# Performance work log

Measured on AMD Instinct MI355X. Metric: run time of the kernel, lower is better.

The kernel has to match this reference:

```python
import jax, jax.numpy as jnp
import numpy as np

B, S, E, H = 2, 2048, 1024, 16
D = E // H  # head_dim = 64
TRIL = D * (D + 1) // 2  # 2080


def setup_inputs() -> dict:
    key = jax.random.key(0)
    ks = jax.random.split(key, 6)
    return {
        "x": jax.random.normal(ks[0], (B, S, E), dtype=jnp.float32),
        "params": jax.random.normal(ks[1], (H, TRIL), dtype=jnp.float32),
        "Wv": jax.random.normal(ks[2], (E, E), dtype=jnp.float32) * 0.02,
        "bv": jax.random.normal(ks[3], (E,), dtype=jnp.float32) * 0.02,
        "Wo": jax.random.normal(ks[4], (E, E), dtype=jnp.float32) * 0.02,
        "bo": jax.random.normal(ks[5], (E,), dtype=jnp.float32) * 0.02,
    }


def reference(x, params, Wv, bv, Wo, bo):
    # x: [B,S,E]; 'symmetry' modification, dropout in eval mode (identity).
    bs, seq_len, emb_dim = x.shape
    d = D
    rows, cols = jnp.tril_indices(d)  # row-major, matches torch.tril_indices
    # Build per-head lower-triangular factor then symmetric PSD Wqk = L @ L^T.
    tril = jnp.zeros((H, d, d), dtype=x.dtype).at[:, rows, cols].set(params)
    Wqk = jnp.einsum('hij,hkj->hik', tril, tril)  # [H,d,d]
    xh = x.reshape(bs, seq_len, H, d)             # [B,S,H,d]
    # scores[b,h,s,t] = x_s^T Wqk_h x_t / sqrt(d)
    t = jnp.einsum('bshd,hde->bshe', xh, Wqk)
    scores = jnp.einsum('bshe,bthe->bhst', t, xh) / jnp.sqrt(jnp.asarray(d, x.dtype))
    attn = jax.nn.softmax(scores, axis=-1)        # [B,H,S,S]
    Vh = (x @ Wv.T + bv).reshape(bs, seq_len, H, d)
    out = jnp.einsum('bhst,bthd->bshd', attn, Vh).reshape(bs, seq_len, emb_dim)
    return out @ Wo.T + bo
```

## Files before the change

kernel.cpp:

```cpp
#include <hip/hip_runtime.h>
#include <math.h>

static constexpr int kB = 2;
static constexpr int kS = 2048;
static constexpr int kE = 1024;
static constexpr int kH = 16;
static constexpr int kD = 64;
static constexpr int kTRIL = 2080;

typedef __attribute__((ext_vector_type(8))) _Float16 f16x8;
typedef __attribute__((ext_vector_type(4))) _Float16 f16x4;
typedef __attribute__((ext_vector_type(2))) __fp16 fp16x2;
typedef __attribute__((ext_vector_type(4))) float f32x4;
typedef __attribute__((ext_vector_type(16))) float f32x16;
typedef __attribute__((ext_vector_type(4))) unsigned int u32x4;
typedef __attribute__((ext_vector_type(2))) unsigned int u32x2;

__device__ __forceinline__ void split_f16(float f, _Float16& hi, _Float16& lo) {
    hi = (_Float16)f;
    lo = (_Float16)(f - (float)hi);
}

__device__ __forceinline__ void gload_lds16(const void* g, void* l) {
    __builtin_amdgcn_global_load_lds(
        (const __attribute__((address_space(1))) unsigned int*)g,
        (__attribute__((address_space(3))) unsigned int*)l, 16, 0, 0);
}

__device__ __forceinline__ unsigned pack_f16(float a, float b) {
    fp16x2 p = __builtin_amdgcn_cvt_pkrtz(a, b);
    return __builtin_bit_cast(unsigned, p);
}

__device__ __forceinline__ unsigned partner32(unsigned x, int hi) {
    u32x2 r = __builtin_amdgcn_permlane32_swap(x, x, false, false);
    return hi ? r[0] : r[1];
}
__device__ __forceinline__ float partner32_f(float x, int hi) {
    return __builtin_bit_cast(float, partner32(__builtin_bit_cast(unsigned, x), hi));
}

__device__ __forceinline__ float max3f(float a, float b, float c) {
    return fmaxf(fmaxf(a, b), c);
}

__global__ __launch_bounds__(256) void setup_kernel(
    const float* __restrict__ Wv, const float* __restrict__ Wo,
    const float* __restrict__ x, const float* __restrict__ params,
    _Float16* __restrict__ wvf, _Float16* __restrict__ wof,
    _Float16* __restrict__ xf,
    _Float16* __restrict__ wqkh, _Float16* __restrict__ wqkl)
{
    const int bid = blockIdx.x;
    if (bid < 2048) {
        const int half = bid >> 10;
        const int i = (bid & 1023) * 256 + threadIdx.x;
        const float* src = half ? Wo : Wv;
        _Float16* dst = half ? wof : wvf;
        const float4 v = ((const float4*)src)[i];
        f16x4 o = {(_Float16)v.x, (_Float16)v.y, (_Float16)v.z, (_Float16)v.w};
        ((f16x4*)dst)[i] = o;
        return;
    }
    if (bid < 6144) {
        const int i = (bid - 2048) * 256 + threadIdx.x;
        const float4 v = ((const float4*)x)[i];
        f16x4 o = {(_Float16)v.x, (_Float16)v.y, (_Float16)v.z, (_Float16)v.w};
        ((f16x4*)xf)[i] = o;
        return;
    }
    __shared__ float p[kTRIL];
    const int h = bid - 6144;
    for (int i = threadIdx.x; i < kTRIL; i += 256) p[i] = params[h * kTRIL + i];
    __syncthreads();
    for (int idx = threadIdx.x; idx < kD * kD; idx += 256) {
        const int i = idx >> 6;
        const int j = idx & 63;
        const int m = i < j ? i : j;
        const float* pi = p + (i * (i + 1)) / 2;
        const float* pj = p + (j * (j + 1)) / 2;
        float s = 0.f;
        for (int k = 0; k <= m; ++k) s += pi[k] * pj[k];
        _Float16 a, b;
        split_f16(s, a, b);
        wqkh[h * kD * kD + idx] = a;
        wqkl[h * kD * kD + idx] = b;
    }
}

__global__ __launch_bounds__(256) void mid_kernel(
    const _Float16* __restrict__ xf, const _Float16* __restrict__ wvf,
    const float* __restrict__ bv, _Float16* __restrict__ VtG,
    const _Float16* __restrict__ wqkh, const _Float16* __restrict__ wqkl,
    _Float16* __restrict__ Qhf, _Float16* __restrict__ Qlf)
{
    __shared__ char arena[65536];
    const int tid = threadIdx.x;
    const int w = tid >> 6, l = tid & 63;
    const int srow = 8 * w + (l >> 3);
    const int cpos = l & 7;

    if (blockIdx.x < 256) {
        _Float16 (*Ab)[128 * 64] = (_Float16 (*)[128 * 64])arena;
        _Float16 (*Bb)[128 * 64] = (_Float16 (*)[128 * 64])(arena + 32768);
        const int K_ = kE;
        const int g = l >> 4, lm = l & 15;
        const int wm = w >> 1, wn = w & 1;
        const int bm = (blockIdx.x >> 3) * 128, bn = (blockIdx.x & 7) * 128;

        f32x4 acc[4][4];
#pragma unroll
        for (int i = 0; i < 4; ++i)
#pragma unroll
            for (int j = 0; j < 4; ++j) acc[i][j] = (f32x4){0.f, 0.f, 0.f, 0.f};

        auto stage = [&](int buf, int k0) {
#pragma unroll
            for (int j = 0; j < 4; ++j) {
                const int r = 32 * j + srow;
                const int c = cpos ^ (r & 7);
                gload_lds16(xf + (size_t)(bm + r) * K_ + k0 + c * 8, &Ab[buf][j * 2048 + w * 512]);
                gload_lds16(wvf + (size_t)(bn + r) * K_ + k0 + c * 8, &Bb[buf][j * 2048 + w * 512]);
            }
        };

        stage(0, 0);
        __syncthreads();
        int cur = 0;
        const int NT = K_ / 64;
        for (int t = 0; t < NT; ++t) {
            if (t + 1 < NT) stage(cur ^ 1, 64 * (t + 1));
            f16x8 a[4][2], bf[4][2];
#pragma unroll
            for (int i = 0; i < 4; ++i) {
                const int rA = wm * 64 + i * 16 + lm;
                const int rB = wn * 64 + i * 16 + lm;
#pragma unroll
                for (int ks = 0; ks < 2; ++ks) {
                    a[i][ks]  = *(const f16x8*)&Ab[cur][rA * 64 + (((4 * ks + g) ^ (rA & 7)) * 8)];
                    bf[i][ks] = *(const f16x8*)&Bb[cur][rB * 64 + (((4 * ks + g) ^ (rB & 7)) * 8)];
                }
            }
            __builtin_amdgcn_s_setprio(1);
#pragma unroll
            for (int ks = 0; ks < 2; ++ks)
#pragma unroll
                for (int mi = 0; mi < 4; ++mi)
#pragma unroll
                    for (int ni = 0; ni < 4; ++ni)
                        acc[mi][ni] = __builtin_amdgcn_mfma_f32_16x16x32_f16(
                            a[mi][ks], bf[ni][ks], acc[mi][ni], 0, 0, 0);
            __builtin_amdgcn_s_setprio(0);
            __syncthreads();
            cur ^= 1;
        }

#pragma unroll
        for (int ni = 0; ni < 4; ++ni) {
            const int col = bn + wn * 64 + ni * 16 + lm;
            const float bb = bv[col];
            const int hh = col >> 6, dd = col & 63;
#pragma unroll
            for (int mi = 0; mi < 4; ++mi) {
                const int tok = bm + wm * 64 + mi * 16 + g * 4;
                const int b = tok >> 11, s0 = tok & 2047;
                f16x4 pk;
#pragma unroll
                for (int r = 0; r < 4; ++r) pk[r] = (_Float16)(acc[mi][ni][r] + bb);
                *(f16x4*)(VtG + ((size_t)(b * kH + hh) * kD + dd) * kS + s0) = pk;
            }
        }
    } else {
        _Float16* Wh = (_Float16*)arena;
        _Float16* Wl = (_Float16*)(arena + 8192);
        const int wk = blockIdx.x - 256;
        const int b = wk >> 8;
        const int h = (wk >> 4) & 15;
        const int tg = wk & 15;
        const int hi = l >> 5;
        const int lq = l & 31;

#pragma unroll
        for (int j = 0; j < 2; ++j) {
            const int r = 32 * j + srow;
            const int c = cpos ^ (r & 7);
            gload_lds16(wqkh + (size_t)(h * kD + r) * kD + c * 8, &Wh[j * 2048 + w * 512]);
            gload_lds16(wqkl + (size_t)(h * kD + r) * kD + c * 8, &Wl[j * 2048 + w * 512]);
        }

        const int tok = tg * 128 + 32 * w + lq;
        f16x8 xq[4];
        {
            const size_t xoff = ((size_t)(b * kS + tok)) * kE + h * kD + 8 * hi;
#pragma unroll
            for (int ks = 0; ks < 4; ++ks)
                xq[ks] = *(const f16x8*)(xf + xoff + 16 * ks);
        }
        f32x16 acc[2];
#pragma unroll
        for (int r = 0; r < 16; ++r) { acc[0][r] = 0.f; acc[1][r] = 0.f; }
        __syncthreads();

#pragma unroll
        for (int et = 0; et < 2; ++et) {
            const int r = 32 * et + lq;
            const int rb = r * 64;
            const int rsw = r & 7;
#pragma unroll
            for (int ks = 0; ks < 4; ++ks) {
                const int cd = 2 * ks + hi;
                f16x8 wh = *(const f16x8*)&Wh[rb + ((cd ^ rsw) * 8)];
                f16x8 wl = *(const f16x8*)&Wl[rb + ((cd ^ rsw) * 8)];
                acc[et] = __builtin_amdgcn_mfma_f32_32x32x16_f16(wh, xq[ks], acc[et], 0, 0, 0);
                acc[et] = __builtin_amdgcn_mfma_f32_32x32x16_f16(wl, xq[ks], acc[et], 0, 0, 0);
            }
        }

        const float sc = 0.125f * 1.44269504088896340736f;
        const size_t qbase = ((size_t)(b * kS + tok)) * kE + h * kD;
#pragma unroll
        for (int et = 0; et < 2; ++et)
#pragma unroll
            for (int m = 0; m < 4; ++m) {
                const int e0 = 32 * et + 8 * m + 4 * hi;
                f16x4 hv, lv;
#pragma unroll
                for (int j = 0; j < 4; ++j) {
                    _Float16 a, c;
                    split_f16(acc[et][4 * m + j] * sc, a, c);
                    hv[j] = a; lv[j] = c;
                }
                *(f16x4*)(Qhf + qbase + e0) = hv;
                *(f16x4*)(Qlf + qbase + e0) = lv;
            }
    }
}

__global__ __launch_bounds__(256) void gemm_out(
    const _Float16* __restrict__ A, const _Float16* __restrict__ Bw,
    const float* __restrict__ bias, float* __restrict__ C,
    int M, int N, int K)
{
    __shared__ _Float16 Ab[2][128 * 64];
    __shared__ _Float16 Bb[2][128 * 64];

    const int tid = threadIdx.x;
    const int w = tid >> 6, l = tid & 63;
    const int g = l >> 4, lm = l & 15;
    const int wm = w >> 1, wn = w & 1;
    const int bm = blockIdx.y * 128, bn = blockIdx.x * 128;
    const int srow = 8 * w + (l >> 3);
    const int cp = l & 7;

    f32x4 acc[4][4];
#pragma unroll
    for (int i = 0; i < 4; ++i)
#pragma unroll
        for (int j = 0; j < 4; ++j) acc[i][j] = (f32x4){0.f, 0.f, 0.f, 0.f};

    auto stage = [&](int buf, int k0) {
#pragma unroll
        for (int j = 0; j < 4; ++j) {
            const int r = 32 * j + srow;
            const int c = cp ^ (r & 7);
            gload_lds16(A + (size_t)(bm + r) * K + k0 + c * 8, &Ab[buf][j * 2048 + w * 512]);
            gload_lds16(Bw + (size_t)(bn + r) * K + k0 + c * 8, &Bb[buf][j * 2048 + w * 512]);
        }
    };

    stage(0, 0);
    __syncthreads();
    int cur = 0;
    const int NT = K / 64;
    for (int t = 0; t < NT; ++t) {
        if (t + 1 < NT) stage(cur ^ 1, 64 * (t + 1));
        f16x8 a[4][2], bf[4][2];
#pragma unroll
        for (int i = 0; i < 4; ++i) {
            const int rA = wm * 64 + i * 16 + lm;
            const int rB = wn * 64 + i * 16 + lm;
#pragma unroll
            for (int ks = 0; ks < 2; ++ks) {
                a[i][ks]  = *(const f16x8*)&Ab[cur][rA * 64 + (((4 * ks + g) ^ (rA & 7)) * 8)];
                bf[i][ks] = *(const f16x8*)&Bb[cur][rB * 64 + (((4 * ks + g) ^ (rB & 7)) * 8)];
            }
        }
        __builtin_amdgcn_s_setprio(1);
#pragma unroll
        for (int ks = 0; ks < 2; ++ks)
#pragma unroll
            for (int mi = 0; mi < 4; ++mi)
#pragma unroll
                for (int ni = 0; ni < 4; ++ni)
                    acc[mi][ni] = __builtin_amdgcn_mfma_f32_16x16x32_f16(
                        a[mi][ks], bf[ni][ks], acc[mi][ni], 0, 0, 0);
        __builtin_amdgcn_s_setprio(0);
        __syncthreads();
        cur ^= 1;
    }

    float bv4[4];
#pragma unroll
    for (int ni = 0; ni < 4; ++ni) bv4[ni] = bias[bn + wn * 64 + ni * 16 + lm];
#pragma unroll
    for (int mi = 0; mi < 4; ++mi) {
        const int row0 = bm + wm * 64 + mi * 16 + g * 4;
#pragma unroll
        for (int r = 0; r < 4; ++r) {
            float* crow = C + (size_t)(row0 + r) * N;
#pragma unroll
            for (int ni = 0; ni < 4; ++ni)
                crow[bn + wn * 64 + ni * 16 + lm] = acc[mi][ni][r] + bv4[ni];
        }
    }
}

__global__ __launch_bounds__(256, 2) void flash_attn_mfma(
    const _Float16* __restrict__ Qhf, const _Float16* __restrict__ Qlf,
    const _Float16* __restrict__ xf, const _Float16* __restrict__ VtG,
    _Float16* __restrict__ AO)
{
    __shared__ _Float16 Kf[2][64 * 64];
    __shared__ _Float16 Vts[2][64 * 64];

    const int tid = threadIdx.x;
    const int l = tid & 63;
    const int w = tid >> 6;
    const int hi = l >> 5;
    const int lq = l & 31;

    const int s = blockIdx.x + 16 * blockIdx.y + 256 * blockIdx.z;
    const int wk = (s & 7) * 64 + (s >> 3);
    const int q0 = (wk & 15) * 128;
    const int h = (wk >> 4) & 15;
    const int b = wk >> 8;
    const int tdiag = (wk & 15) * 2;

    f16x8 qh[4], ql[4];
    {
        const size_t qoff = ((size_t)(b * kS + q0 + 32 * w + lq)) * kE + h * kD + 8 * hi;
#pragma unroll
        for (int ks = 0; ks < 4; ++ks) {
            qh[ks] = *(const f16x8*)(Qhf + qoff + 16 * ks);
            ql[ks] = *(const f16x8*)(Qlf + qoff + 16 * ks);
        }
    }
    f16x8 ones;
#pragma unroll
    for (int j = 0; j < 8; ++j) ones[j] = (_Float16)1.0f;

    f32x16 oacc[2], lacc;
#pragma unroll
    for (int r = 0; r < 16; ++r) { oacc[0][r] = 0.f; oacc[1][r] = 0.f; lacc[r] = 0.f; }
    float mrun = -INFINITY;

    const int srow = 8 * w + (l >> 3);
    const int cpos = l & 7;
    const size_t vthead = ((size_t)(b * kH + h) * kD) * kS;
    const size_t xbase = (size_t)(b * kS) * kE + h * kD;

    int koff[2][4];
    int vo[2][2][2];
#pragma unroll
    for (int kt = 0; kt < 2; ++kt) {
        const int key = 32 * kt + lq;
        const int kr = key * 64, ksw = key & 7;
#pragma unroll
        for (int ks = 0; ks < 4; ++ks)
            koff[kt][ks] = kr + (((2 * ks + hi) ^ ksw) * 8);
    }
#pragma unroll
    for (int dt = 0; dt < 2; ++dt) {
        const int d = 32 * dt + lq;
        const int dr = d * 64, dsw = d & 7;
#pragma unroll
        for (int kt = 0; kt < 2; ++kt) {
            vo[dt][kt][0] = dr + (((4 * kt + hi) ^ dsw) * 8);
            vo[dt][kt][1] = dr + (((4 * kt + 2 + hi) ^ dsw) * 8);
        }
    }

    auto stage = [&](int buf, int k0) {
#pragma unroll
        for (int j = 0; j < 2; ++j) {
            const int r = 32 * j + srow;
            const int c = cpos ^ (r & 7);
            gload_lds16(xf + xbase + (size_t)(k0 + r) * kE + c * 8, &Kf[buf][j * 2048 + w * 512]);
            gload_lds16(VtG + vthead + (size_t)r * kS + k0 + c * 8, &Vts[buf][j * 2048 + w * 512]);
        }
    };

    auto tile_body = [&](int curb) {
        f32x16 sacc[2];
#pragma unroll
        for (int r = 0; r < 16; ++r) { sacc[0][r] = 0.f; sacc[1][r] = 0.f; }
        __builtin_amdgcn_s_setprio(1);
#pragma unroll
        for (int ks = 0; ks < 4; ++ks)
#pragma unroll
            for (int kt = 0; kt < 2; ++kt) {
                f16x8 kf = *(const f16x8*)&Kf[curb][koff[kt][ks]];
                sacc[kt] = __builtin_amdgcn_mfma_f32_32x32x16_f16(kf, qh[ks], sacc[kt], 0, 0, 0);
                sacc[kt] = __builtin_amdgcn_mfma_f32_32x32x16_f16(kf, ql[ks], sacc[kt], 0, 0, 0);
            }
        __builtin_amdgcn_s_setprio(0);

        float m0 = max3f(max3f(sacc[0][0], sacc[0][1], sacc[0][2]),
                         max3f(sacc[0][3], sacc[0][4], sacc[0][5]),
                         max3f(sacc[0][6], sacc[0][7], sacc[0][8]));
        float m1 = max3f(max3f(sacc[0][9], sacc[0][10], sacc[0][11]),
                         max3f(sacc[0][12], sacc[0][13], sacc[0][14]),
                         sacc[0][15]);
        float m2 = max3f(max3f(sacc[1][0], sacc[1][1], sacc[1][2]),
                         max3f(sacc[1][3], sacc[1][4], sacc[1][5]),
                         max3f(sacc[1][6], sacc[1][7], sacc[1][8]));
        float m3 = max3f(max3f(sacc[1][9], sacc[1][10], sacc[1][11]),
                         max3f(sacc[1][12], sacc[1][13], sacc[1][14]),
                         sacc[1][15]);
        float tmax = fmaxf(fmaxf(m0, m1), fmaxf(m2, m3));
        tmax = fmaxf(tmax, partner32_f(tmax, hi));

        if (!__any(tmax > mrun - 20.0f)) return;

        if (__any(tmax > mrun + 14.0f)) {
            const float mnew = fmaxf(mrun, tmax);
            const float alpha = exp2f(mrun - mnew);
            oacc[0] *= alpha;
            oacc[1] *= alpha;
            lacc *= alpha;
            mrun = mnew;
        }

#pragma unroll
        for (int kt = 0; kt < 2; ++kt) {
            unsigned wds[8], pw[8];
#pragma unroll
            for (int i = 0; i < 8; ++i) {
                const float p0 = exp2f(sacc[kt][2 * i] - mrun);
                const float p1 = exp2f(sacc[kt][2 * i + 1] - mrun);
                wds[i] = pack_f16(p0, p1);
            }
#pragma unroll
            for (int i = 0; i < 8; ++i) pw[i] = partner32(wds[i], hi);
            u32x4 f0 = hi ? (u32x4){pw[2], pw[3], wds[2], wds[3]}
                          : (u32x4){wds[0], wds[1], pw[0], pw[1]};
            u32x4 f1 = hi ? (u32x4){pw[6], pw[7], wds[6], wds[7]}
                          : (u32x4){wds[4], wds[5], pw[4], pw[5]};
            f16x8 pf0 = __builtin_bit_cast(f16x8, f0);
            f16x8 pf1 = __builtin_bit_cast(f16x8, f1);
            __builtin_amdgcn_s_setprio(1);
            lacc = __builtin_amdgcn_mfma_f32_32x32x16_f16(ones, pf0, lacc, 0, 0, 0);
            lacc = __builtin_amdgcn_mfma_f32_32x32x16_f16(ones, pf1, lacc, 0, 0, 0);
#pragma unroll
            for (int dt = 0; dt < 2; ++dt) {
                f16x8 v0 = *(const f16x8*)&Vts[curb][vo[dt][kt][0]];
                f16x8 v1 = *(const f16x8*)&Vts[curb][vo[dt][kt][1]];
                oacc[dt] = __builtin_amdgcn_mfma_f32_32x32x16_f16(v0, pf0, oacc[dt], 0, 0, 0);
                oacc[dt] = __builtin_amdgcn_mfma_f32_32x32x16_f16(v1, pf1, oacc[dt], 0, 0, 0);
            }
            __builtin_amdgcn_s_setprio(0);
        }
    };

    auto kof = [&](int i) { return ((tdiag + i) & 31) * 64; };

    stage(0, kof(0));
    for (int t = 0; t < 32; t += 2) {
        __syncthreads();
        if (t + 1 < 32) stage(1, kof(t + 1));
        tile_body(0);
        __syncthreads();
        if (t + 2 < 32) stage(0, kof(t + 2));
        tile_body(1);
    }

    const float inv = 1.0f / lacc[0];
    const size_t obase = ((size_t)(b * kS + q0 + 32 * w + lq)) * kE + h * kD;
#pragma unroll
    for (int dt = 0; dt < 2; ++dt)
#pragma unroll
        for (int rr = 0; rr < 4; ++rr) {
            const int d0 = 32 * dt + 8 * rr + 4 * hi;
            f16x4 pk;
#pragma unroll
            for (int j = 0; j < 4; ++j) pk[j] = (_Float16)(oacc[dt][4 * rr + j] * inv);
            *(f16x4*)(AO + obase + d0) = pk;
        }
}

extern "C" void kernel_launch(void* const* d_in, const int* in_sizes, int n_in,
                              void* d_out, int out_size, void* d_ws, size_t ws_size,
                              hipStream_t stream) {
    (void)in_sizes; (void)n_in; (void)out_size; (void)ws_size;
    const float* x      = (const float*)d_in[0];
    const float* params = (const float*)d_in[1];
    const float* Wv     = (const float*)d_in[2];
    const float* bv     = (const float*)d_in[3];
    const float* Wo     = (const float*)d_in[4];
    const float* bo     = (const float*)d_in[5];
    float* out = (float*)d_out;

    const size_t NE = (size_t)kB * kS * kE;
    const size_t NW = (size_t)kE * kE;
    const size_t NQ = (size_t)kH * kD * kD;

    char* ws = (char*)d_ws;
    size_t off = 0;
    _Float16* wqkh = (_Float16*)(ws + off); off += NQ * 2;
    _Float16* wqkl = (_Float16*)(ws + off); off += NQ * 2;
    _Float16* xf   = (_Float16*)(ws + off); off += NE * 2;
    _Float16* wvf  = (_Float16*)(ws + off); off += NW * 2;
    _Float16* wof  = (_Float16*)(ws + off); off += NW * 2;
    _Float16* Qhf  = (_Float16*)(ws + off); off += NE * 2;
    _Float16* Qlf  = (_Float16*)(ws + off); off += NE * 2;
    _Float16* VtG  = (_Float16*)(ws + off); off += NE * 2;
    _Float16* AO   = (_Float16*)(ws + off); off += NE * 2;

    setup_kernel<<<6160, 256, 0, stream>>>(Wv, Wo, x, params, wvf, wof, xf, wqkh, wqkl);
    mid_kernel<<<768, 256, 0, stream>>>(xf, wvf, bv, VtG, wqkh, wqkl, Qhf, Qlf);
    flash_attn_mfma<<<dim3(kS / 128, kH, kB), 256, 0, stream>>>(Qhf, Qlf, xf, VtG, AO);
    gemm_out<<<dim3(kE / 128, (kB * kS) / 128), 256, 0, stream>>>(
        AO, wof, bo, out, kB * kS, kE, kE);
}
```

Baseline: 117.8 us.

## Skip key tiles whose Cauchy-Schwarz score bound is negligible versus the diagonal

Because Wqk is positive semidefinite, each query's own diagonal score is m_s, and sqrt(m_s*m_t) bounds its score against key t. The mid kernel now writes sqrt(m_s) per token and a per-tile maximum via atomicMax. The attention kernel uses these to build a mask of key tiles that can still reach within 2^-18 of the diagonal score. It then streams only those tiles with a ctz-driven double-buffered loop, removing most QK/PV MFMA work and K/V loads when scores are dominated by the diagonal. In exchange it adds a reduction and atomics in the mid kernel and a block-wide mask computation, and it introduces a small bounded approximation error from the dropped tiles.

New measurement: 120.0 us. No clear change (+1.9%).

```diff
diff --git a/kernel.cpp b/kernel.cpp
--- a/kernel.cpp
+++ b/kernel.cpp
@@ -49,7 +49,8 @@
     const float* __restrict__ x, const float* __restrict__ params,
     _Float16* __restrict__ wvf, _Float16* __restrict__ wof,
     _Float16* __restrict__ xf,
-    _Float16* __restrict__ wqkh, _Float16* __restrict__ wqkl)
+    _Float16* __restrict__ wqkh, _Float16* __restrict__ wqkl,
+    int* __restrict__ tmaxrootI)
 {
     const int bid = blockIdx.x;
     if (bid < 2048) {
@@ -67,6 +68,10 @@
         const float4 v = ((const float4*)x)[i];
         f16x4 o = {(_Float16)v.x, (_Float16)v.y, (_Float16)v.z, (_Float16)v.w};
         ((f16x4*)xf)[i] = o;
+        return;
+    }
+    if (bid == 6160) {
+        for (int i = threadIdx.x; i < kB * kH * 32; i += 256) tmaxrootI[i] = 0;
         return;
     }
     __shared__ float p[kTRIL];
@@ -92,7 +97,8 @@
     const _Float16* __restrict__ xf, const _Float16* __restrict__ wvf,
     const float* __restrict__ bv, _Float16* __restrict__ VtG,
     const _Float16* __restrict__ wqkh, const _Float16* __restrict__ wqkl,
-    _Float16* __restrict__ Qhf, _Float16* __restrict__ Qlf)
+    _Float16* __restrict__ Qhf, _Float16* __restrict__ Qlf,
+    float* __restrict__ rootm, int* __restrict__ tmaxrootI)
 {
     __shared__ char arena[65536];
     const int tid = threadIdx.x;
@@ -218,6 +224,29 @@
 
         const float sc = 0.125f * 1.44269504088896340736f;
         const size_t qbase = ((size_t)(b * kS + tok)) * kE + h * kD;
+
+        float dotp = 0.f;
+#pragma unroll
+        for (int et = 0; et < 2; ++et)
+#pragma unroll
+            for (int m = 0; m < 4; ++m) {
+                f16x4 xv = *(const f16x4*)(xf + qbase + 32 * et + 8 * m + 4 * hi);
+#pragma unroll
+                for (int j = 0; j < 4; ++j)
+                    dotp += acc[et][4 * m + j] * (float)xv[j];
+            }
+        const float dfull = dotp + partner32_f(dotp, hi);
+        const float mdiag = dfull * sc;
+        const float rv = sqrtf(fmaxf(mdiag, 0.f));
+        if (!hi) rootm[((size_t)(b * kH + h)) * kS + tok] = rv;
+        float wmax = rv;
+#pragma unroll
+        for (int mask = 1; mask < 64; mask <<= 1)
+            wmax = fmaxf(wmax, __shfl_xor(wmax, mask));
+        if (l == 0)
+            atomicMax(&tmaxrootI[(b * kH + h) * 32 + 2 * tg + (w >> 1)],
+                      __float_as_int(wmax));
+
 #pragma unroll
         for (int et = 0; et < 2; ++et)
 #pragma unroll
@@ -318,10 +347,12 @@
 __global__ __launch_bounds__(256, 2) void flash_attn_mfma(
     const _Float16* __restrict__ Qhf, const _Float16* __restrict__ Qlf,
     const _Float16* __restrict__ xf, const _Float16* __restrict__ VtG,
+    const float* __restrict__ rootm, const int* __restrict__ tmaxrootI,
     _Float16* __restrict__ AO)
 {
     __shared__ _Float16 Kf[2][64 * 64];
     __shared__ _Float16 Vts[2][64 * 64];
+    __shared__ unsigned wmaskS[4];
 
     const int tid = threadIdx.x;
     const int l = tid & 63;
@@ -358,6 +389,10 @@
     const int cpos = l & 7;
     const size_t vthead = ((size_t)(b * kH + h) * kD) * kS;
     const size_t xbase = (size_t)(b * kS) * kE + h * kD;
+
+    const float rootm_q = rootm[((size_t)(b * kH + h)) * kS + q0 + 32 * w + lq];
+    const float mdiag_q = rootm_q * rootm_q;
+    const float* trt = (const float*)(tmaxrootI + (b * kH + h) * 32);
 
     int koff[2][4];
     int vo[2][2][2];
@@ -462,17 +497,30 @@
         }
     };
 
-    auto kof = [&](int i) { return ((tdiag + i) & 31) * 64; };
-
-    stage(0, kof(0));
-    for (int t = 0; t < 32; t += 2) {
+    unsigned msk = 0;
+    for (int tb = 0; tb < 32; ++tb) {
+        const float bound = rootm_q * trt[tb];
+        if (__any(bound > mdiag_q - 18.0f)) msk |= (1u << tb);
+    }
+    msk |= (3u << tdiag);
+    wmaskS[w] = msk;
+    __syncthreads();
+    msk = wmaskS[0] | wmaskS[1] | wmaskS[2] | wmaskS[3];
+
+    unsigned rm = (msk >> tdiag) | (tdiag ? (msk << (32 - tdiag)) : 0u);
+
+    int i0 = __builtin_ctz(rm); rm &= rm - 1;
+    stage(0, ((tdiag + i0) & 31) * 64);
+    int buf = 0;
+    __syncthreads();
+    while (rm) {
+        const int in = __builtin_ctz(rm); rm &= rm - 1;
+        stage(buf ^ 1, ((tdiag + in) & 31) * 64);
+        tile_body(buf);
         __syncthreads();
-        if (t + 1 < 32) stage(1, kof(t + 1));
-        tile_body(0);
-        __syncthreads();
-        if (t + 2 < 32) stage(0, kof(t + 2));
-        tile_body(1);
-    }
+        buf ^= 1;
+    }
+    tile_body(buf);
 
     const float inv = 1.0f / lacc[0];
     const size_t obase = ((size_t)(b * kS + q0 + 32 * w + lq)) * kE + h * kD;
@@ -503,6 +551,7 @@
     const size_t NE = (size_t)kB * kS * kE;
     const size_t NW = (size_t)kE * kE;
     const size_t NQ = (size_t)kH * kD * kD;
+    const size_t NS = (size_t)kB * kH * kS;
 
     char* ws = (char*)d_ws;
     size_t off = 0;
@@ -515,10 +564,15 @@
     _Float16* Qlf  = (_Float16*)(ws + off); off += NE * 2;
     _Float16* VtG  = (_Float16*)(ws + off); off += NE * 2;
     _Float16* AO   = (_Float16*)(ws + off); off += NE * 2;
-
-    setup_kernel<<<6160, 256, 0, stream>>>(Wv, Wo, x, params, wvf, wof, xf, wqkh, wqkl);
-    mid_kernel<<<768, 256, 0, stream>>>(xf, wvf, bv, VtG, wqkh, wqkl, Qhf, Qlf);
-    flash_attn_mfma<<<dim3(kS / 128, kH, kB), 256, 0, stream>>>(Qhf, Qlf, xf, VtG, AO);
+    float*    rootm     = (float*)(ws + off); off += NS * 4;
+    int*      tmaxrootI = (int*)(ws + off);   off += (size_t)kB * kH * 32 * 4;
+
+    setup_kernel<<<6161, 256, 0, stream>>>(Wv, Wo, x, params, wvf, wof, xf,
+                                           wqkh, wqkl, tmaxrootI);
+    mid_kernel<<<768, 256, 0, stream>>>(xf, wvf, bv, VtG, wqkh, wqkl,
+                                        Qhf, Qlf, rootm, tmaxrootI);
+    flash_attn_mfma<<<dim3(kS / 128, kH, kB), 256, 0, stream>>>(
+        Qhf, Qlf, xf, VtG, rootm, tmaxrootI, AO);
     gemm_out<<<dim3(kE / 128, (kB * kS) / 128), 256, 0, stream>>>(
         AO, wof, bo, out, kB * kS, kE, kE);
 }
```

## Split key range across two wave groups per block and merge softmax partials

Applied to the files above, without the earlier changes.

Doubles the attention block to 512 threads. Each half of the waves processes 16 of the 32 key tiles into its own double-buffered LDS region. Half 0 shares its running max early so half 1 starts from a better max estimate, and at the end the two partial (max, sum, output) states are combined through LDS before the normalized store. The aim is to raise per-CU wave occupancy and shorten each wave's serial key loop, at the cost of more LDS, an extra combine step and tighter register limits from the new launch bounds.

New measurement: 154.5 us. +31.1%, slower.

```diff
diff --git a/kernel.cpp b/kernel.cpp
--- a/kernel.cpp
+++ b/kernel.cpp
@@ -315,19 +315,24 @@
     }
 }
 
-__global__ __launch_bounds__(256, 2) void flash_attn_mfma(
+__global__ __launch_bounds__(512, 4) void flash_attn_mfma(
     const _Float16* __restrict__ Qhf, const _Float16* __restrict__ Qlf,
     const _Float16* __restrict__ xf, const _Float16* __restrict__ VtG,
     _Float16* __restrict__ AO)
 {
-    __shared__ _Float16 Kf[2][64 * 64];
-    __shared__ _Float16 Vts[2][64 * 64];
+    __shared__ char smem[66048];
 
     const int tid = threadIdx.x;
     const int l = tid & 63;
     const int w = tid >> 6;
+    const int half = w >> 2;
+    const int wq = w & 3;
     const int hi = l >> 5;
     const int lq = l & 31;
+
+    _Float16* Kf  = (_Float16*)(smem + half * 32768);
+    _Float16* Vts = (_Float16*)(smem + half * 32768 + 16384);
+    float* mtmp = (float*)(smem + 65536);
 
     const int s = blockIdx.x + 16 * blockIdx.y + 256 * blockIdx.z;
     const int wk = (s & 7) * 64 + (s >> 3);
@@ -338,7 +343,7 @@
 
     f16x8 qh[4], ql[4];
     {
-        const size_t qoff = ((size_t)(b * kS + q0 + 32 * w + lq)) * kE + h * kD + 8 * hi;
+        const size_t qoff = ((size_t)(b * kS + q0 + 32 * wq + lq)) * kE + h * kD + 8 * hi;
 #pragma unroll
         for (int ks = 0; ks < 4; ++ks) {
             qh[ks] = *(const f16x8*)(Qhf + qoff + 16 * ks);
@@ -354,7 +359,7 @@
     for (int r = 0; r < 16; ++r) { oacc[0][r] = 0.f; oacc[1][r] = 0.f; lacc[r] = 0.f; }
     float mrun = -INFINITY;
 
-    const int srow = 8 * w + (l >> 3);
+    const int srow = 8 * wq + (l >> 3);
     const int cpos = l & 7;
     const size_t vthead = ((size_t)(b * kH + h) * kD) * kS;
     const size_t xbase = (size_t)(b * kS) * kE + h * kD;
@@ -380,17 +385,32 @@
         }
     }
 
+    auto kof = [&](int i) { return ((tdiag + 16 * half + i) & 31) * 64; };
+
     auto stage = [&](int buf, int k0) {
 #pragma unroll
         for (int j = 0; j < 2; ++j) {
             const int r = 32 * j + srow;
             const int c = cpos ^ (r & 7);
-            gload_lds16(xf + xbase + (size_t)(k0 + r) * kE + c * 8, &Kf[buf][j * 2048 + w * 512]);
-            gload_lds16(VtG + vthead + (size_t)r * kS + k0 + c * 8, &Vts[buf][j * 2048 + w * 512]);
+            gload_lds16(xf + xbase + (size_t)(k0 + r) * kE + c * 8,
+                        Kf + buf * 4096 + j * 2048 + wq * 512);
+            gload_lds16(VtG + vthead + (size_t)r * kS + k0 + c * 8,
+                        Vts + buf * 4096 + j * 2048 + wq * 512);
         }
     };
 
+    auto merge_max = [&](float mext) {
+        const float mnew = fmaxf(mrun, mext);
+        const float alpha = exp2f(mrun - mnew);
+        oacc[0] *= alpha;
+        oacc[1] *= alpha;
+        lacc *= alpha;
+        mrun = mnew;
+    };
+
     auto tile_body = [&](int curb) {
+        const _Float16* kb = Kf + curb * 4096;
+        const _Float16* vb = Vts + curb * 4096;
         f32x16 sacc[2];
 #pragma unroll
         for (int r = 0; r < 16; ++r) { sacc[0][r] = 0.f; sacc[1][r] = 0.f; }
@@ -399,7 +419,7 @@
         for (int ks = 0; ks < 4; ++ks)
 #pragma unroll
             for (int kt = 0; kt < 2; ++kt) {
-                f16x8 kf = *(const f16x8*)&Kf[curb][koff[kt][ks]];
+                f16x8 kf = *(const f16x8*)&kb[koff[kt][ks]];
                 sacc[kt] = __builtin_amdgcn_mfma_f32_32x32x16_f16(kf, qh[ks], sacc[kt], 0, 0, 0);
                 sacc[kt] = __builtin_amdgcn_mfma_f32_32x32x16_f16(kf, ql[ks], sacc[kt], 0, 0, 0);
             }
@@ -422,14 +442,7 @@
 
         if (!__any(tmax > mrun - 20.0f)) return;
 
-        if (__any(tmax > mrun + 14.0f)) {
-            const float mnew = fmaxf(mrun, tmax);
-            const float alpha = exp2f(mrun - mnew);
-            oacc[0] *= alpha;
-            oacc[1] *= alpha;
-            lacc *= alpha;
-            mrun = mnew;
-        }
+        if (__any(tmax > mrun + 14.0f)) merge_max(tmax);
 
 #pragma unroll
         for (int kt = 0; kt < 2; ++kt) {
@@ -453,8 +466,8 @@
             lacc = __builtin_amdgcn_mfma_f32_32x32x16_f16(ones, pf1, lacc, 0, 0, 0);
 #pragma unroll
             for (int dt = 0; dt < 2; ++dt) {
-                f16x8 v0 = *(const f16x8*)&Vts[curb][vo[dt][kt][0]];
-                f16x8 v1 = *(const f16x8*)&Vts[curb][vo[dt][kt][1]];
+                f16x8 v0 = *(const f16x8*)&vb[vo[dt][kt][0]];
+                f16x8 v1 = *(const f16x8*)&vb[vo[dt][kt][1]];
                 oacc[dt] = __builtin_amdgcn_mfma_f32_32x32x16_f16(v0, pf0, oacc[dt], 0, 0, 0);
                 oacc[dt] = __builtin_amdgcn_mfma_f32_32x32x16_f16(v1, pf1, oacc[dt], 0, 0, 0);
             }
@@ -462,30 +475,52 @@
         }
     };
 
-    auto kof = [&](int i) { return ((tdiag + i) & 31) * 64; };
-
     stage(0, kof(0));
-    for (int t = 0; t < 32; t += 2) {
+    for (int t = 0; t < 16; ++t) {
         __syncthreads();
-        if (t + 1 < 32) stage(1, kof(t + 1));
-        tile_body(0);
-        __syncthreads();
-        if (t + 2 < 32) stage(0, kof(t + 2));
-        tile_body(1);
-    }
-
-    const float inv = 1.0f / lacc[0];
-    const size_t obase = ((size_t)(b * kS + q0 + 32 * w + lq)) * kE + h * kD;
-#pragma unroll
-    for (int dt = 0; dt < 2; ++dt)
-#pragma unroll
-        for (int rr = 0; rr < 4; ++rr) {
-            const int d0 = 32 * dt + 8 * rr + 4 * hi;
-            f16x4 pk;
-#pragma unroll
-            for (int j = 0; j < 4; ++j) pk[j] = (_Float16)(oacc[dt][4 * rr + j] * inv);
-            *(f16x4*)(AO + obase + d0) = pk;
-        }
+        if (t + 1 < 16) stage((t + 1) & 1, kof(t + 1));
+        if (t == 2 && half == 1)
+            merge_max(mtmp[wq * 32 + lq]);
+        tile_body(t & 1);
+        if (t == 1 && half == 0 && hi == 0)
+            mtmp[wq * 32 + lq] = mrun;
+    }
+
+    __syncthreads();
+    float* comb = (float*)smem;
+    const int cbase = (wq * 64 + l) * 34;
+    if (half == 1) {
+        comb[cbase] = mrun;
+        comb[cbase + 1] = lacc[0];
+#pragma unroll
+        for (int j = 0; j < 16; ++j) {
+            comb[cbase + 2 + j] = oacc[0][j];
+            comb[cbase + 18 + j] = oacc[1][j];
+        }
+    }
+    __syncthreads();
+    if (half == 0) {
+        const float mB = comb[cbase];
+        const float lB = comb[cbase + 1];
+        const float mS = fmaxf(mrun, mB);
+        const float aA = exp2f(mrun - mS);
+        const float aB = exp2f(mB - mS);
+        const float inv = 1.0f / (lacc[0] * aA + lB * aB);
+        const size_t obase = ((size_t)(b * kS + q0 + 32 * wq + lq)) * kE + h * kD;
+#pragma unroll
+        for (int dt = 0; dt < 2; ++dt)
+#pragma unroll
+            for (int rr = 0; rr < 4; ++rr) {
+                const int d0 = 32 * dt + 8 * rr + 4 * hi;
+                f16x4 pk;
+#pragma unroll
+                for (int j = 0; j < 4; ++j) {
+                    const float ob = comb[cbase + 2 + 16 * dt + 4 * rr + j];
+                    pk[j] = (_Float16)((oacc[dt][4 * rr + j] * aA + ob * aB) * inv);
+                }
+                *(f16x4*)(AO + obase + d0) = pk;
+            }
+    }
 }
 
 extern "C" void kernel_launch(void* const* d_in, const int* in_sizes, int n_in,
@@ -518,7 +553,7 @@
 
     setup_kernel<<<6160, 256, 0, stream>>>(Wv, Wo, x, params, wvf, wof, xf, wqkh, wqkl);
     mid_kernel<<<768, 256, 0, stream>>>(xf, wvf, bv, VtG, wqkh, wqkl, Qhf, Qlf);
-    flash_attn_mfma<<<dim3(kS / 128, kH, kB), 256, 0, stream>>>(Qhf, Qlf, xf, VtG, AO);
+    flash_attn_mfma<<<dim3(kS / 128, kH, kB), 512, 0, stream>>>(Qhf, Qlf, xf, VtG, AO);
     gemm_out<<<dim3(kE / 128, (kB * kS) / 128), 256, 0, stream>>>(
         AO, wof, bo, out, kB * kS, kE, kE);
 }
```
